# Optimization experiments

Measured on AMD Instinct MI355X. Metric: run time of the kernel, lower is better.

The kernel has to match this reference:

```python
import jax, jax.numpy as jnp
import numpy as np

B, S, D, H, HD = 2, 2048, 2048, 16, 128


def precompute_freqs_cis(dim, end, theta=10000.0):
    freqs = 1.0 / theta ** (np.arange(0, dim, 2, dtype=np.float32)[: dim // 2] / dim)
    t = np.arange(end, dtype=np.float32)
    freqs = np.outer(t, freqs)
    freqs = np.concatenate((freqs, freqs), axis=-1)  # [S, HD]
    return jnp.asarray(np.cos(freqs)), jnp.asarray(np.sin(freqs))


def rotate_half(x):
    x1, x2 = x[..., : x.shape[-1] // 2], x[..., x.shape[-1] // 2 :]
    return jnp.concatenate((-x2, x1), axis=-1)


def setup_inputs() -> dict:
    key = jax.random.key(0)
    ks = jax.random.split(key, 5)
    scale = 1.0 / np.sqrt(D)
    return {
        "x": jax.random.normal(ks[0], (B, S, D), jnp.float32),
        "mask": jnp.ones((1, 1, S, S), jnp.bool_),
        "Wq": jax.random.normal(ks[1], (D, H, HD), jnp.float32) * scale,
        "Wk": jax.random.normal(ks[2], (D, H, HD), jnp.float32) * scale,
        "Wv": jax.random.normal(ks[3], (D, H, HD), jnp.float32) * scale,
        "Wo": jax.random.normal(ks[4], (H, HD, D), jnp.float32) * scale,
    }


def reference(x, mask, Wq, Wk, Wv, Wo):
    seq_len = x.shape[1]
    head_dim = Wq.shape[-1]
    # QKV projections: [B,S,D] x [D,H,HD] -> [B,S,H,HD]
    q = jnp.einsum("bsd,dhk->bshk", x, Wq)
    k = jnp.einsum("bsd,dhk->bshk", x, Wk)
    v = jnp.einsum("bsd,dhk->bshk", x, Wv)
    # Rotary position embedding
    cos, sin = precompute_freqs_cis(head_dim, seq_len)
    cos = cos[None, :, None, :]  # [1,S,1,HD]
    sin = sin[None, :, None, :]
    q = q * cos + rotate_half(q) * sin
    k = k * cos + rotate_half(k) * sin
    # Scaled dot-product attention (flax dot_product_attention semantics)
    scores = jnp.einsum("bqhk,bskh->bhqs", q / jnp.sqrt(jnp.float32(head_dim)), k.swapaxes(-1, -2))
    big_neg = jnp.finfo(scores.dtype).min
    scores = jnp.where(mask, scores, big_neg)
    attn = jax.nn.softmax(scores, axis=-1)  # [B,H,S,S]
    ctx = jnp.einsum("bhqs,bshk->bqhk", attn, v)  # [B,S,H,HD]
    # Output projection over (head, head_dim)
    return jnp.einsum("bqhk,hkd->bqd", ctx, Wo)
```

## Files before the change

kernel.cpp:

```cpp
#include <hip/hip_runtime.h>
#include <math.h>

#define Bc   2
#define Sc   2048
#define Dc   2048
#define Hc   16
#define HDc  128
#define BSc  4096
#define HHDc 2048

typedef __bf16 bf16_t;
typedef __bf16 bf16x8 __attribute__((ext_vector_type(8)));
typedef __bf16 bf16x4 __attribute__((ext_vector_type(4)));
typedef float  f32x4  __attribute__((ext_vector_type(4)));

#define AS1(p) ((const __attribute__((address_space(1))) void*)(p))
#define AS3(p) ((__attribute__((address_space(3))) void*)(p))

#define MFMA16(a,b,c) __builtin_amdgcn_mfma_f32_16x16x32_bf16((a),(b),(c),0,0,0)

__global__ void convert_x(const float* __restrict__ x, bf16_t* __restrict__ xb)
{
    const size_t i = ((size_t)blockIdx.x * 256 + threadIdx.x) * 4;
    float4 v = *(const float4*)&x[i];
    bf16x4 o; o[0]=(bf16_t)v.x; o[1]=(bf16_t)v.y; o[2]=(bf16_t)v.z; o[3]=(bf16_t)v.w;
    *(bf16x4*)&xb[i] = o;
}

__global__ __launch_bounds__(256) void transpose_w(const float* __restrict__ in,
                                                   bf16_t* __restrict__ out)
{
    __shared__ float T[64][65];
    const int t = threadIdx.x;
    const int r0 = blockIdx.y * 64, c0 = blockIdx.x * 64;
    #pragma unroll
    for (int i = 0; i < 4; ++i) {
        int row = i * 16 + (t >> 4);
        int c4  = (t & 15) * 4;
        float4 v = *(const float4*)&in[(size_t)(r0 + row) * 2048 + c0 + c4];
        T[row][c4] = v.x; T[row][c4+1] = v.y; T[row][c4+2] = v.z; T[row][c4+3] = v.w;
    }
    __syncthreads();
    #pragma unroll
    for (int i = 0; i < 4; ++i) {
        int orow = i * 16 + (t >> 4);
        int c4   = (t & 15) * 4;
        bf16x4 o;
        #pragma unroll
        for (int j = 0; j < 4; ++j) o[j] = (bf16_t)T[c4 + j][orow];
        *(bf16x4*)&out[(size_t)(c0 + orow) * 2048 + r0 + c4] = o;
    }
}

__global__ void rope_tab(float* __restrict__ tab)
{
    const int i = blockIdx.x * 256 + threadIdx.x;
    const int j = i & 63, s = i >> 6;
    const float freq = expf(-(float)j * 0.14391156514261520f);
    float sn, cs;
    sincosf((float)s * freq, &sn, &cs);
    float2 v; v.x = cs; v.y = sn;
    *(float2*)&tab[i * 2] = v;
}

template<int MS, int NS>
__device__ __forceinline__ void mf_quad(f32x4 (&acc)[8][4],
                                        const bf16x8 (&a)[4][2],
                                        const bf16x8 (&b)[2][2])
{
    #pragma unroll
    for (int ks = 0; ks < 2; ++ks)
        #pragma unroll
        for (int mf = 0; mf < 4; ++mf)
            #pragma unroll
            for (int nf = 0; nf < 2; ++nf)
                acc[MS * 4 + mf][NS * 2 + nf] =
                    MFMA16(a[mf][ks], b[nf][ks], acc[MS * 4 + mf][NS * 2 + nf]);
}

__global__ __launch_bounds__(512, 2) void qkv_gemm8(const bf16_t* __restrict__ A,
                                                    const bf16_t* __restrict__ Bt,
                                                    float* __restrict__ Qf,
                                                    float* __restrict__ Kf,
                                                    bf16_t* __restrict__ Vt)
{
    __shared__ bf16_t As[2][256 * 64];
    __shared__ bf16_t Bs[2][256 * 64];

    const int t = threadIdx.x;
    const int w = t >> 6, l = t & 63;
    const int wm = w >> 2, wn = w & 3;
    const int lane15 = l & 15, quad = l >> 4;
    const int swr = (lane15 & 7) * 8;
    const int m0 = blockIdx.y * 256, n0 = blockIdx.x * 256;

    const int gk = (((l & 7) ^ ((l >> 3) & 7)) * 8);

    auto stageA = [&](int buf, int h, int kt) {
        #pragma unroll
        for (int p = 0; p < 2; ++p) {
            const int rb = p * 128 + h * 64 + w * 8;
            __builtin_amdgcn_global_load_lds(
                AS1(A + (size_t)(m0 + rb + (l >> 3)) * 2048 + kt * 64 + gk),
                AS3(&As[buf][rb * 64]), 16, 0, 0);
        }
    };
    auto stageB = [&](int buf, int h, int kt) {
        #pragma unroll
        for (int p = 0; p < 2; ++p) {
            const int rb = (2 * p + (w >> 2)) * 64 + h * 32 + (w & 3) * 8;
            __builtin_amdgcn_global_load_lds(
                AS1(Bt + (size_t)(n0 + rb + (l >> 3)) * 2048 + kt * 64 + gk),
                AS3(&Bs[buf][rb * 64]), 16, 0, 0);
        }
    };

    bf16x8 a[4][2], b[2][2];
    auto rdA = [&](int buf, int msub) {
        #pragma unroll
        for (int mf = 0; mf < 4; ++mf)
            #pragma unroll
            for (int ks = 0; ks < 2; ++ks) {
                const int ra = wm * 128 + msub * 64 + mf * 16 + lane15;
                a[mf][ks] = *(const bf16x8*)&As[buf][ra * 64 + (((ks * 4 + quad) * 8) ^ swr)];
            }
    };
    auto rdB = [&](int buf, int nsub) {
        #pragma unroll
        for (int nf = 0; nf < 2; ++nf)
            #pragma unroll
            for (int ks = 0; ks < 2; ++ks) {
                const int rb = wn * 64 + nsub * 32 + nf * 16 + lane15;
                b[nf][ks] = *(const bf16x8*)&Bs[buf][rb * 64 + (((ks * 4 + quad) * 8) ^ swr)];
            }
    };

    f32x4 acc[8][4];
    #pragma unroll
    for (int i = 0; i < 8; ++i)
        #pragma unroll
        for (int j = 0; j < 4; ++j)
            #pragma unroll
            for (int c = 0; c < 4; ++c) acc[i][j][c] = 0.f;

    stageA(0, 0, 0); stageB(0, 0, 0); stageB(0, 1, 0); stageA(0, 1, 0);

    for (int kt = 0; kt < 31; ++kt) {
        const int cur = kt & 1, nxt = cur ^ 1;
        asm volatile("s_waitcnt vmcnt(4)" ::: "memory");
        __builtin_amdgcn_s_barrier();
        __builtin_amdgcn_sched_barrier(0);
        stageA(nxt, 0, kt + 1);
        rdA(cur, 0); rdB(cur, 0);
        __builtin_amdgcn_s_setprio(1); mf_quad<0,0>(acc, a, b); __builtin_amdgcn_s_setprio(0);
        asm volatile("s_waitcnt vmcnt(4)" ::: "memory");
        __builtin_amdgcn_s_barrier();
        __builtin_amdgcn_sched_barrier(0);
        stageB(nxt, 0, kt + 1);
        rdB(cur, 1);
        __builtin_amdgcn_s_setprio(1); mf_quad<0,1>(acc, a, b); __builtin_amdgcn_s_setprio(0);
        asm volatile("s_waitcnt vmcnt(4)" ::: "memory");
        __builtin_amdgcn_s_barrier();
        __builtin_amdgcn_sched_barrier(0);
        stageB(nxt, 1, kt + 1);
        rdA(cur, 1); rdB(cur, 0);
        __builtin_amdgcn_s_setprio(1); mf_quad<1,0>(acc, a, b); __builtin_amdgcn_s_setprio(0);
        __builtin_amdgcn_s_barrier();
        stageA(nxt, 1, kt + 1);
        rdB(cur, 1);
        __builtin_amdgcn_s_setprio(1); mf_quad<1,1>(acc, a, b); __builtin_amdgcn_s_setprio(0);
    }
    asm volatile("s_waitcnt vmcnt(0)" ::: "memory");
    __builtin_amdgcn_s_barrier();
    __builtin_amdgcn_sched_barrier(0);
    rdA(1, 0); rdB(1, 0); mf_quad<0,0>(acc, a, b);
    rdB(1, 1);            mf_quad<0,1>(acc, a, b);
    rdA(1, 1); rdB(1, 0); mf_quad<1,0>(acc, a, b);
    rdB(1, 1);            mf_quad<1,1>(acc, a, b);

    if (n0 < 4096) {
        float* __restrict__ dst = (n0 < 2048) ? Qf : Kf;
        const int nb = n0 & 2047;
        #pragma unroll
        for (int msub = 0; msub < 2; ++msub)
            #pragma unroll
            for (int mf = 0; mf < 4; ++mf)
                #pragma unroll
                for (int nsub = 0; nsub < 2; ++nsub)
                    #pragma unroll
                    for (int nf = 0; nf < 2; ++nf)
                        #pragma unroll
                        for (int r = 0; r < 4; ++r) {
                            const int gm = m0 + wm * 128 + msub * 64 + mf * 16 + quad * 4 + r;
                            const int gn = nb + wn * 64 + nsub * 32 + nf * 16 + lane15;
                            dst[(size_t)gm * 2048 + gn] = acc[msub * 4 + mf][nsub * 2 + nf][r];
                        }
    } else {
        const int nb = n0 - 4096;
        #pragma unroll
        for (int msub = 0; msub < 2; ++msub)
            #pragma unroll
            for (int mf = 0; mf < 4; ++mf) {
                const int gm = m0 + wm * 128 + msub * 64 + mf * 16 + quad * 4;
                const int bq = gm >> 11;
                const int s  = gm & 2047;
                #pragma unroll
                for (int nsub = 0; nsub < 2; ++nsub)
                    #pragma unroll
                    for (int nf = 0; nf < 2; ++nf) {
                        const int gn = nb + wn * 64 + nsub * 32 + nf * 16 + lane15;
                        const int h  = gn >> 7, hd = gn & 127;
                        bf16x4 o;
                        #pragma unroll
                        for (int r = 0; r < 4; ++r)
                            o[r] = (bf16_t)acc[msub * 4 + mf][nsub * 2 + nf][r];
                        *(bf16x4*)&Vt[((size_t)((bq * Hc + h) * HDc + hd)) * Sc + s] = o;
                    }
            }
    }
}

__global__ __launch_bounds__(256) void gemm_bt(const bf16_t* __restrict__ A,
                                               const bf16_t* __restrict__ Bt,
                                               float* __restrict__ C)
{
    __shared__ bf16_t As[128 * 64];
    __shared__ bf16_t Bs[128 * 64];
    const int t = threadIdx.x;
    const int w = t >> 6, l = t & 63;
    const int wm = w >> 1, wn = w & 1;
    const int lane15 = l & 15, quad = l >> 4;
    const int swr = (lane15 & 7) * 8;
    const int m0 = blockIdx.y * 128, n0 = blockIdx.x * 128;

    f32x4 acc[4][4];
    #pragma unroll
    for (int i = 0; i < 4; ++i)
        #pragma unroll
        for (int j = 0; j < 4; ++j)
            #pragma unroll
            for (int c = 0; c < 4; ++c) acc[i][j][c] = 0.f;

    const int srow = w * 8 + (l >> 3);
    const int gk   = ((l & 7) * 8) ^ ((srow & 7) * 8);

    for (int k0 = 0; k0 < 2048; k0 += 64) {
        __syncthreads();
        #pragma unroll
        for (int p = 0; p < 4; ++p) {
            __builtin_amdgcn_global_load_lds(
                AS1(A + (size_t)(m0 + p * 32 + srow) * 2048 + k0 + gk),
                AS3(&As[(p * 32 + w * 8) * 64]), 16, 0, 0);
            __builtin_amdgcn_global_load_lds(
                AS1(Bt + (size_t)(n0 + p * 32 + srow) * 2048 + k0 + gk),
                AS3(&Bs[(p * 32 + w * 8) * 64]), 16, 0, 0);
        }
        __syncthreads();
        #pragma unroll
        for (int ks = 0; ks < 2; ++ks) {
            const int rc = ((ks * 4 + quad) * 8) ^ swr;
            bf16x8 a[4], b[4];
            #pragma unroll
            for (int mt = 0; mt < 4; ++mt)
                a[mt] = *(const bf16x8*)&As[(wm * 64 + mt * 16 + lane15) * 64 + rc];
            #pragma unroll
            for (int nt = 0; nt < 4; ++nt)
                b[nt] = *(const bf16x8*)&Bs[(wn * 64 + nt * 16 + lane15) * 64 + rc];
            #pragma unroll
            for (int mt = 0; mt < 4; ++mt)
                #pragma unroll
                for (int nt = 0; nt < 4; ++nt)
                    acc[mt][nt] = MFMA16(a[mt], b[nt], acc[mt][nt]);
        }
    }

    #pragma unroll
    for (int mt = 0; mt < 4; ++mt)
        #pragma unroll
        for (int nt = 0; nt < 4; ++nt)
            #pragma unroll
            for (int r = 0; r < 4; ++r) {
                const int gm = m0 + wm * 64 + mt * 16 + quad * 4 + r;
                const int gn = n0 + wn * 64 + nt * 16 + lane15;
                C[(size_t)gm * 2048 + gn] = acc[mt][nt][r];
            }
}

__global__ void rope_scale_cast(const float* __restrict__ Qf,
                                const float* __restrict__ Kf,
                                const float* __restrict__ tab,
                                bf16_t* __restrict__ Qh,
                                bf16_t* __restrict__ Kh)
{
    const int idx  = blockIdx.x * 256 + threadIdx.x;
    const int j4   = (idx & 15) * 4;
    const int h    = (idx >> 4) & (Hc - 1);
    const int sabs = idx >> 8;
    const int s    = sabs & (Sc - 1);
    const float QS = 0.08838834764831845f;

    const size_t base = (size_t)sabs * HHDc + (size_t)h * HDc + j4;
    float4 q1 = *(const float4*)&Qf[base];
    float4 q2 = *(const float4*)&Qf[base + 64];
    float4 k1 = *(const float4*)&Kf[base];
    float4 k2 = *(const float4*)&Kf[base + 64];
    float4 t0 = *(const float4*)&tab[(s * 64 + j4) * 2];
    float4 t1 = *(const float4*)&tab[(s * 64 + j4 + 2) * 2];

    bf16x4 qo1, qo2, ko1, ko2;
    #pragma unroll
    for (int c = 0; c < 4; ++c) {
        const float cs = (c < 2) ? ((c & 1) ? t0.z : t0.x) : ((c & 1) ? t1.z : t1.x);
        const float sn = (c < 2) ? ((c & 1) ? t0.w : t0.y) : ((c & 1) ? t1.w : t1.y);
        const float a = ((const float*)&q1)[c], bq = ((const float*)&q2)[c];
        const float x = ((const float*)&k1)[c], y  = ((const float*)&k2)[c];
        qo1[c] = (bf16_t)((a * cs - bq * sn) * QS);
        qo2[c] = (bf16_t)((bq * cs + a * sn) * QS);
        ko1[c] = (bf16_t)(x * cs - y * sn);
        ko2[c] = (bf16_t)(y * cs + x * sn);
    }
    *(bf16x4*)&Qh[base]      = qo1;
    *(bf16x4*)&Qh[base + 64] = qo2;
    *(bf16x4*)&Kh[base]      = ko1;
    *(bf16x4*)&Kh[base + 64] = ko2;
}

__global__ __launch_bounds__(512, 4) void attn_v7(const bf16_t* __restrict__ Q,
                                                  const bf16_t* __restrict__ K,
                                                  const bf16_t* __restrict__ Vt,
                                                  bf16_t* __restrict__ CTX)
{
    __shared__ bf16_t Ks[64 * 128];
    __shared__ bf16_t Vts[128 * 64];
    __shared__ bf16_t Ps[128 * 72];

    const int t = threadIdx.x, w = t >> 6, l = t & 63;
    const int lane15 = l & 15, quad = l >> 4;
    const int swr = (lane15 & 7) * 8;
    const int q0 = blockIdx.x * 128;
    const int b = blockIdx.y >> 4, h = blockIdx.y & 15;
    const size_t qbase = ((size_t)(b * Sc + q0)) * HHDc + h * HDc;
    const size_t vtb   = (size_t)blockIdx.y * HDc * Sc;
    const size_t kb0   = ((size_t)(b * Sc)) * HHDc + h * HDc;

    bf16x8 qf[4];
    #pragma unroll
    for (int ks = 0; ks < 4; ++ks)
        qf[ks] = *(const bf16x8*)&Q[qbase
            + (size_t)(w * 16 + lane15) * HHDc + (ks * 4 + quad) * 8];

    float m_ = -INFINITY, l_ = 0.f;

    f32x4 O[8];
    #pragma unroll
    for (int i = 0; i < 8; ++i)
        #pragma unroll
        for (int c = 0; c < 4; ++c) O[i][c] = 0.f;

    const int krow0 = w * 4 + (l >> 4);
    const int kgc   = lane15 * 8;
    const int vrow0 = w * 8 + (l >> 3);
    const int vgc   = (l & 7) * 8;

    bf16x8 kst[2], vst[2];
    #pragma unroll
    for (int p = 0; p < 2; ++p) {
        kst[p] = *(const bf16x8*)&K[kb0 + (size_t)(p * 32 + krow0) * HHDc + kgc];
        vst[p] = *(const bf16x8*)&Vt[vtb + (size_t)(p * 64 + vrow0) * Sc + vgc];
    }

    for (int kt = 0; kt < Sc / 64; ++kt) {
        __syncthreads();
        #pragma unroll
        for (int p = 0; p < 2; ++p) {
            const int rk = p * 32 + krow0;
            *(bf16x8*)&Ks[rk * 128 + (kgc ^ ((rk & 7) * 8))] = kst[p];
        }
        #pragma unroll
        for (int p = 0; p < 2; ++p) {
            const int rv = p * 64 + vrow0;
            *(bf16x8*)&Vts[rv * 64 + (vgc ^ ((rv & 7) * 8))] = vst[p];
        }
        if (kt + 1 < Sc / 64) {
            const size_t kbn = kb0 + (size_t)(kt + 1) * 64 * HHDc;
            #pragma unroll
            for (int p = 0; p < 2; ++p) {
                kst[p] = *(const bf16x8*)&K[kbn + (size_t)(p * 32 + krow0) * HHDc + kgc];
                vst[p] = *(const bf16x8*)&Vt[vtb + (size_t)(p * 64 + vrow0) * Sc
                                             + (kt + 1) * 64 + vgc];
            }
        }
        __syncthreads();

        f32x4 sc[4];
        #pragma unroll
        for (int j = 0; j < 4; ++j)
            #pragma unroll
            for (int c = 0; c < 4; ++c) sc[j][c] = 0.f;
        __builtin_amdgcn_s_setprio(1);
        #pragma unroll
        for (int ks = 0; ks < 4; ++ks) {
            const int rc = ((ks * 4 + quad) * 8) ^ swr;
            bf16x8 bk[4];
            #pragma unroll
            for (int nt = 0; nt < 4; ++nt)
                bk[nt] = *(const bf16x8*)&Ks[(nt * 16 + lane15) * 128 + rc];
            #pragma unroll
            for (int nt = 0; nt < 4; ++nt)
                sc[nt] = MFMA16(bk[nt], qf[ks], sc[nt]);
        }
        __builtin_amdgcn_s_setprio(0);

        {
            float tm = -INFINITY;
            #pragma unroll
            for (int nt = 0; nt < 4; ++nt)
                #pragma unroll
                for (int r = 0; r < 4; ++r) tm = fmaxf(tm, sc[nt][r]);
            tm = fmaxf(tm, __shfl_xor(tm, 16));
            tm = fmaxf(tm, __shfl_xor(tm, 32));
            const float mo = m_;
            const float mn = fmaxf(mo, tm);
            const float al = __expf(mo - mn);
            m_ = mn;
            float ts = 0.f;
            const int prow = (w * 16 + lane15) * 72;
            #pragma unroll
            for (int nt = 0; nt < 4; ++nt) {
                bf16x4 pw;
                #pragma unroll
                for (int r = 0; r < 4; ++r) {
                    const float p = __expf(sc[nt][r] - mn);
                    pw[r] = (bf16_t)p;
                    ts += p;
                }
                *(bf16x4*)&Ps[prow + nt * 16 + quad * 4] = pw;
            }
            ts += __shfl_xor(ts, 16);
            ts += __shfl_xor(ts, 32);
            l_ = l_ * al + ts;

            #pragma unroll
            for (int ht = 0; ht < 8; ++ht)
                #pragma unroll
                for (int c = 0; c < 4; ++c) O[ht][c] *= al;
        }

        __builtin_amdgcn_s_setprio(1);
        #pragma unroll
        for (int ks = 0; ks < 2; ++ks) {
            const int rcp = (ks * 4 + quad) * 8;
            const int rcv = rcp ^ swr;
            bf16x8 av[8];
            #pragma unroll
            for (int ht = 0; ht < 8; ++ht)
                av[ht] = *(const bf16x8*)&Vts[(ht * 16 + lane15) * 64 + rcv];
            bf16x8 bp = *(const bf16x8*)&Ps[(w * 16 + lane15) * 72 + rcp];
            #pragma unroll
            for (int ht = 0; ht < 8; ++ht)
                O[ht] = MFMA16(av[ht], bp, O[ht]);
        }
        __builtin_amdgcn_s_setprio(0);
    }

    {
        const float linv = 1.0f / l_;
        const int s = q0 + w * 16 + lane15;
        #pragma unroll
        for (int ht = 0; ht < 8; ++ht) {
            bf16x4 o;
            #pragma unroll
            for (int c = 0; c < 4; ++c) o[c] = (bf16_t)(O[ht][c] * linv);
            *(bf16x4*)&CTX[((size_t)(b * Sc + s)) * HHDc + h * HDc + ht * 16 + quad * 4] = o;
        }
    }
}

extern "C" void kernel_launch(void* const* d_in, const int* in_sizes, int n_in,
                              void* d_out, int out_size, void* d_ws, size_t ws_size,
                              hipStream_t stream)
{
    const float* x  = (const float*)d_in[0];
    const float* Wq = (const float*)d_in[2];
    const float* Wk = (const float*)d_in[3];
    const float* Wv = (const float*)d_in[4];
    const float* Wo = (const float*)d_in[5];
    float* out = (float*)d_out;

    bf16_t* W0  = (bf16_t*)d_ws;
    bf16_t* xb  = W0;
    bf16_t* WT3 = W0 + 8388608;
    bf16_t* WoT = W0 + 20971520;
    float*  Qf  = (float*)(W0 + 25165824);
    float*  Kf  = (float*)(W0 + 41943040);
    bf16_t* Vt  = W0 + 58720256;
    bf16_t* Kh  = W0;
    bf16_t* Qh  = W0 + 8388608;
    bf16_t* CTX = W0 + 25165824;
    float*  tab = out;

    dim3 tw(32, 32);

    rope_tab<<<512, 256, 0, stream>>>(tab);
    convert_x<<<8192, 256, 0, stream>>>(x, xb);
    transpose_w<<<tw, 256, 0, stream>>>(Wq, WT3);
    transpose_w<<<tw, 256, 0, stream>>>(Wk, WT3 + 4194304);
    transpose_w<<<tw, 256, 0, stream>>>(Wv, WT3 + 8388608);
    transpose_w<<<tw, 256, 0, stream>>>(Wo, WoT);

    qkv_gemm8<<<dim3(24, 16), 512, 0, stream>>>(xb, WT3, Qf, Kf, Vt);

    rope_scale_cast<<<4096, 256, 0, stream>>>(Qf, Kf, tab, Qh, Kh);

    attn_v7<<<dim3(16, 32), 512, 0, stream>>>(Qh, Kh, Vt, CTX);

    gemm_bt<<<dim3(16, 32), 256, 0, stream>>>(CTX, WoT, out);
}
```

Measured before the change: 469.7 us.

## Fuse RoPE, scale and bf16 cast into QKV GEMM epilogue with reworked pipeline

Removes the separate rope_scale_cast kernel. The QKV GEMM now applies rotary embedding, the query scale and the bf16 cast in its epilogue, which avoids writing fp32 Q/K to global memory and reading them back. To make each lane hold both halves of a rotary pair, B rows are permuted during staging. The main loop is also restructured into a deeper prefetch schedule with barriers around every MFMA phase. The extra barriers and the strided bf16 scalar stores in the epilogue could add overhead.

```diff
diff --git a/kernel.cpp b/kernel.cpp
--- a/kernel.cpp
+++ b/kernel.cpp
@@ -78,11 +78,21 @@
                     MFMA16(a[mf][ks], b[nf][ks], acc[MS * 4 + mf][NS * 2 + nf]);
 }
 
-__global__ __launch_bounds__(512, 2) void qkv_gemm8(const bf16_t* __restrict__ A,
-                                                    const bf16_t* __restrict__ Bt,
-                                                    float* __restrict__ Qf,
-                                                    float* __restrict__ Kf,
-                                                    bf16_t* __restrict__ Vt)
+#define SBAR() __builtin_amdgcn_sched_barrier(0)
+
+#define PHASE_CORE(MS, NS) \
+    SBAR(); __builtin_amdgcn_s_barrier(); SBAR(); \
+    __builtin_amdgcn_s_setprio(1); \
+    mf_quad<MS, NS>(acc, a, b); \
+    __builtin_amdgcn_s_setprio(0); \
+    SBAR(); __builtin_amdgcn_s_barrier(); SBAR();
+
+__global__ __launch_bounds__(512, 2) void qkv_gemm8r(const bf16_t* __restrict__ A,
+                                                     const bf16_t* __restrict__ Bt,
+                                                     const float* __restrict__ tab,
+                                                     bf16_t* __restrict__ Qh,
+                                                     bf16_t* __restrict__ Kh,
+                                                     bf16_t* __restrict__ Vt)
 {
     __shared__ bf16_t As[2][256 * 64];
     __shared__ bf16_t Bs[2][256 * 64];
@@ -93,13 +103,14 @@
     const int lane15 = l & 15, quad = l >> 4;
     const int swr = (lane15 & 7) * 8;
     const int m0 = blockIdx.y * 256, n0 = blockIdx.x * 256;
+    const bool qk = (n0 < 4096);
 
     const int gk = (((l & 7) ^ ((l >> 3) & 7)) * 8);
 
     auto stageA = [&](int buf, int h, int kt) {
         #pragma unroll
         for (int p = 0; p < 2; ++p) {
-            const int rb = p * 128 + h * 64 + w * 8;
+            const int rb = h * 128 + p * 64 + w * 8;
             __builtin_amdgcn_global_load_lds(
                 AS1(A + (size_t)(m0 + rb + (l >> 3)) * 2048 + kt * 64 + gk),
                 AS3(&As[buf][rb * 64]), 16, 0, 0);
@@ -108,9 +119,12 @@
     auto stageB = [&](int buf, int h, int kt) {
         #pragma unroll
         for (int p = 0; p < 2; ++p) {
-            const int rb = (2 * p + (w >> 2)) * 64 + h * 32 + (w & 3) * 8;
+            const int rb   = h * 128 + p * 64 + w * 8;
+            const int r127 = p * 64 + w * 8 + (l >> 3);
+            const int srow = qk ? ((r127 & 15) | ((r127 >> 1) & 0x30) | ((r127 & 16) << 2))
+                                : r127;
             __builtin_amdgcn_global_load_lds(
-                AS1(Bt + (size_t)(n0 + rb + (l >> 3)) * 2048 + kt * 64 + gk),
+                AS1(Bt + (size_t)(n0 + h * 128 + srow) * 2048 + kt * 64 + gk),
                 AS3(&Bs[buf][rb * 64]), 16, 0, 0);
         }
     };
@@ -144,57 +158,65 @@
             for (int c = 0; c < 4; ++c) acc[i][j][c] = 0.f;
 
     stageA(0, 0, 0); stageB(0, 0, 0); stageB(0, 1, 0); stageA(0, 1, 0);
-
-    for (int kt = 0; kt < 31; ++kt) {
-        const int cur = kt & 1, nxt = cur ^ 1;
+    stageA(1, 0, 1); stageB(1, 0, 1);
+    SBAR();
+    asm volatile("s_waitcnt vmcnt(4)" ::: "memory");
+    __builtin_amdgcn_s_barrier();
+    SBAR();
+
+    for (int T = 0; T < 30; ++T) {
+        const int cur = T & 1, nxt = cur ^ 1;
+        rdA(cur, 0); rdB(cur, 0);
+        stageB(nxt, 1, T + 1);
+        PHASE_CORE(0, 0)
+        rdB(cur, 1);
+        stageA(nxt, 1, T + 1);
+        PHASE_CORE(0, 1)
+        rdA(cur, 1); rdB(cur, 0);
+        stageA(cur, 0, T + 2);
+        PHASE_CORE(1, 0)
+        rdB(cur, 1);
+        stageB(cur, 0, T + 2);
+        SBAR();
         asm volatile("s_waitcnt vmcnt(4)" ::: "memory");
-        __builtin_amdgcn_s_barrier();
-        __builtin_amdgcn_sched_barrier(0);
-        stageA(nxt, 0, kt + 1);
-        rdA(cur, 0); rdB(cur, 0);
-        __builtin_amdgcn_s_setprio(1); mf_quad<0,0>(acc, a, b); __builtin_amdgcn_s_setprio(0);
-        asm volatile("s_waitcnt vmcnt(4)" ::: "memory");
-        __builtin_amdgcn_s_barrier();
-        __builtin_amdgcn_sched_barrier(0);
-        stageB(nxt, 0, kt + 1);
-        rdB(cur, 1);
-        __builtin_amdgcn_s_setprio(1); mf_quad<0,1>(acc, a, b); __builtin_amdgcn_s_setprio(0);
-        asm volatile("s_waitcnt vmcnt(4)" ::: "memory");
-        __builtin_amdgcn_s_barrier();
-        __builtin_amdgcn_sched_barrier(0);
-        stageB(nxt, 1, kt + 1);
-        rdA(cur, 1); rdB(cur, 0);
-        __builtin_amdgcn_s_setprio(1); mf_quad<1,0>(acc, a, b); __builtin_amdgcn_s_setprio(0);
-        __builtin_amdgcn_s_barrier();
-        stageA(nxt, 1, kt + 1);
-        rdB(cur, 1);
-        __builtin_amdgcn_s_setprio(1); mf_quad<1,1>(acc, a, b); __builtin_amdgcn_s_setprio(0);
-    }
+        PHASE_CORE(1, 1)
+    }
+    rdA(0, 0); rdB(0, 0); stageB(1, 1, 31); PHASE_CORE(0, 0)
+    rdB(0, 1);            stageA(1, 1, 31); PHASE_CORE(0, 1)
+    rdA(0, 1); rdB(0, 0);                   PHASE_CORE(1, 0)
+    rdB(0, 1);
+    SBAR();
     asm volatile("s_waitcnt vmcnt(0)" ::: "memory");
-    __builtin_amdgcn_s_barrier();
-    __builtin_amdgcn_sched_barrier(0);
-    rdA(1, 0); rdB(1, 0); mf_quad<0,0>(acc, a, b);
-    rdB(1, 1);            mf_quad<0,1>(acc, a, b);
-    rdA(1, 1); rdB(1, 0); mf_quad<1,0>(acc, a, b);
-    rdB(1, 1);            mf_quad<1,1>(acc, a, b);
-
-    if (n0 < 4096) {
-        float* __restrict__ dst = (n0 < 2048) ? Qf : Kf;
-        const int nb = n0 & 2047;
+    PHASE_CORE(1, 1)
+    rdA(1, 0); rdB(1, 0); PHASE_CORE(0, 0)
+    rdB(1, 1);            PHASE_CORE(0, 1)
+    rdA(1, 1); rdB(1, 0); PHASE_CORE(1, 0)
+    rdB(1, 1);            PHASE_CORE(1, 1)
+
+    if (qk) {
+        const bool isQ = (n0 < 2048);
+        bf16_t* __restrict__ dst = isQ ? Qh : Kh;
+        const float QS = isQ ? 0.08838834764831845f : 1.0f;
+        const int h = ((n0 & 2047) >> 7) + (wn >> 1);
         #pragma unroll
         for (int msub = 0; msub < 2; ++msub)
             #pragma unroll
             for (int mf = 0; mf < 4; ++mf)
                 #pragma unroll
-                for (int nsub = 0; nsub < 2; ++nsub)
+                for (int r = 0; r < 4; ++r) {
+                    const int gm = m0 + wm * 128 + msub * 64 + mf * 16 + quad * 4 + r;
+                    const int bq = gm >> 11, spos = gm & 2047;
+                    const size_t ob = ((size_t)(bq * Sc + spos)) * HHDc + h * HDc;
                     #pragma unroll
-                    for (int nf = 0; nf < 2; ++nf)
-                        #pragma unroll
-                        for (int r = 0; r < 4; ++r) {
-                            const int gm = m0 + wm * 128 + msub * 64 + mf * 16 + quad * 4 + r;
-                            const int gn = nb + wn * 64 + nsub * 32 + nf * 16 + lane15;
-                            dst[(size_t)gm * 2048 + gn] = acc[msub * 4 + mf][nsub * 2 + nf][r];
-                        }
+                    for (int nsub = 0; nsub < 2; ++nsub) {
+                        const int j = lane15 + nsub * 16 + (wn & 1) * 32;
+                        const float2 cssn = *(const float2*)&tab[(spos * 64 + j) * 2];
+                        const float v0 = acc[msub * 4 + mf][nsub * 2 + 0][r];
+                        const float v1 = acc[msub * 4 + mf][nsub * 2 + 1][r];
+                        dst[ob + j]      = (bf16_t)((v0 * cssn.x - v1 * cssn.y) * QS);
+                        dst[ob + j + 64] = (bf16_t)((v1 * cssn.x + v0 * cssn.y) * QS);
+                    }
+                }
     } else {
         const int nb = n0 - 4096;
         #pragma unroll
@@ -286,45 +308,6 @@
             }
 }
 
-__global__ void rope_scale_cast(const float* __restrict__ Qf,
-                                const float* __restrict__ Kf,
-                                const float* __restrict__ tab,
-                                bf16_t* __restrict__ Qh,
-                                bf16_t* __restrict__ Kh)
-{
-    const int idx  = blockIdx.x * 256 + threadIdx.x;
-    const int j4   = (idx & 15) * 4;
-    const int h    = (idx >> 4) & (Hc - 1);
-    const int sabs = idx >> 8;
-    const int s    = sabs & (Sc - 1);
-    const float QS = 0.08838834764831845f;
-
-    const size_t base = (size_t)sabs * HHDc + (size_t)h * HDc + j4;
-    float4 q1 = *(const float4*)&Qf[base];
-    float4 q2 = *(const float4*)&Qf[base + 64];
-    float4 k1 = *(const float4*)&Kf[base];
-    float4 k2 = *(const float4*)&Kf[base + 64];
-    float4 t0 = *(const float4*)&tab[(s * 64 + j4) * 2];
-    float4 t1 = *(const float4*)&tab[(s * 64 + j4 + 2) * 2];
-
-    bf16x4 qo1, qo2, ko1, ko2;
-    #pragma unroll
-    for (int c = 0; c < 4; ++c) {
-        const float cs = (c < 2) ? ((c & 1) ? t0.z : t0.x) : ((c & 1) ? t1.z : t1.x);
-        const float sn = (c < 2) ? ((c & 1) ? t0.w : t0.y) : ((c & 1) ? t1.w : t1.y);
-        const float a = ((const float*)&q1)[c], bq = ((const float*)&q2)[c];
-        const float x = ((const float*)&k1)[c], y  = ((const float*)&k2)[c];
-        qo1[c] = (bf16_t)((a * cs - bq * sn) * QS);
-        qo2[c] = (bf16_t)((bq * cs + a * sn) * QS);
-        ko1[c] = (bf16_t)(x * cs - y * sn);
-        ko2[c] = (bf16_t)(y * cs + x * sn);
-    }
-    *(bf16x4*)&Qh[base]      = qo1;
-    *(bf16x4*)&Qh[base + 64] = qo2;
-    *(bf16x4*)&Kh[base]      = ko1;
-    *(bf16x4*)&Kh[base + 64] = ko2;
-}
-
 __global__ __launch_bounds__(512, 4) void attn_v7(const bf16_t* __restrict__ Q,
                                                   const bf16_t* __restrict__ K,
                                                   const bf16_t* __restrict__ Vt,
@@ -491,12 +474,10 @@
     bf16_t* xb  = W0;
     bf16_t* WT3 = W0 + 8388608;
     bf16_t* WoT = W0 + 20971520;
-    float*  Qf  = (float*)(W0 + 25165824);
-    float*  Kf  = (float*)(W0 + 41943040);
-    bf16_t* Vt  = W0 + 58720256;
-    bf16_t* Kh  = W0;
-    bf16_t* Qh  = W0 + 8388608;
-    bf16_t* CTX = W0 + 25165824;
+    bf16_t* Qh  = W0 + 25165824;
+    bf16_t* Kh  = W0 + 33554432;
+    bf16_t* Vt  = W0 + 41943040;
+    bf16_t* CTX = W0 + 50331648;
     float*  tab = out;
 
     dim3 tw(32, 32);
@@ -508,9 +489,7 @@
     transpose_w<<<tw, 256, 0, stream>>>(Wv, WT3 + 8388608);
     transpose_w<<<tw, 256, 0, stream>>>(Wo, WoT);
 
-    qkv_gemm8<<<dim3(24, 16), 512, 0, stream>>>(xb, WT3, Qf, Kf, Vt);
-
-    rope_scale_cast<<<4096, 256, 0, stream>>>(Qf, Kf, tab, Qh, Kh);
+    qkv_gemm8r<<<dim3(24, 16), 512, 0, stream>>>(xb, WT3, tab, Qh, Kh, Vt);
 
     attn_v7<<<dim3(16, 32), 512, 0, stream>>>(Qh, Kh, Vt, CTX);
 
```

Result: faster. 443.0 us (-5.7%).
